# Performance work log

Hardware: AMD Instinct MI355X
Metric: run time of the kernel (lower is better)

Reference implementation:

```python
import jax, jax.numpy as jnp
import numpy as np

TEMPERATURE = 0.5

def setup_inputs() -> dict:
    key = jax.random.key(0)
    k1, k2 = jax.random.split(key)
    N, D = 4096, 256
    return {
        "z_i": jax.random.normal(k1, (N, D), dtype=jnp.float32),
        "z_j": jax.random.normal(k2, (N, D), dtype=jnp.float32),
    }

def reference(z_i, z_j):
    N = z_i.shape[0]
    z = jnp.concatenate([z_i, z_j], axis=0)                      # [2N, D]
    # cosine similarity via normalize + GEMM (same math as broadcasted CosineSimilarity)
    zn = z / jnp.linalg.norm(z, axis=-1, keepdims=True)
    sim = (zn @ zn.T) / TEMPERATURE                              # [2N, 2N]
    twoN = 2 * N
    eye = jnp.eye(twoN, dtype=bool)
    labels = jnp.arange(N, dtype=jnp.int32)
    labels = jnp.concatenate([labels, labels])
    pos_mask = (labels[None, :] == labels[:, None]) & (~eye)     # positive pairs, no diagonal
    # removing the diagonal before exp == zeroing exp on the diagonal
    exps = jnp.where(eye, 0.0, jnp.exp(sim))                     # [2N, 2N]
    pos = jnp.sum(jnp.where(pos_mask, exps, 0.0), axis=1)        # [2N]
    denom = jnp.sum(exps, axis=1)                                # [2N]
    loss = -jnp.mean(jnp.log(pos / denom))
    return loss
```

## Files before the change

kernel.cpp:

```cpp
#include <hip/hip_runtime.h>
#include <hip/hip_bf16.h>
#include <hip/hip_fp8.h>

#define TWO_N 8192
#define NHALF 4096
#define D 256
#define NTILE 64
#define BLK_BYTES 32768
static constexpr float INV_T = 2.0f;

typedef __attribute__((ext_vector_type(4))) float f32x4;

#define AS1 __attribute__((address_space(1)))
#define AS3 __attribute__((address_space(3)))

__device__ __forceinline__ unsigned int pack4_e4m3(float a, float b, float c, float d) {
#if __has_builtin(__builtin_amdgcn_cvt_pk_fp8_f32)
    int p = 0;
    p = __builtin_amdgcn_cvt_pk_fp8_f32(a, b, p, false);
    p = __builtin_amdgcn_cvt_pk_fp8_f32(c, d, p, true);
    return (unsigned int)p;
#else
    __hip_fp8_e4m3 qa(a), qb(b), qc(c), qd(d);
    return (unsigned int)qa.__x | ((unsigned int)qb.__x << 8) |
           ((unsigned int)qc.__x << 16) | ((unsigned int)qd.__x << 24);
#endif
}

__global__ __launch_bounds__(256) void norm_pos_kernel(
        const float* __restrict__ z_i, const float* __restrict__ z_j,
        unsigned char* __restrict__ znb, float* __restrict__ sim_pos,
        float* __restrict__ denom) {
    const int wid = threadIdx.x >> 6, lane = threadIdx.x & 63;
    const int i = blockIdx.x * 4 + wid;
    const float4 vi = *reinterpret_cast<const float4*>(z_i + (size_t)i * D + lane * 4);
    const float4 vj = *reinterpret_cast<const float4*>(z_j + (size_t)i * D + lane * 4);
    float ssi = vi.x * vi.x + vi.y * vi.y + vi.z * vi.z + vi.w * vi.w;
    float ssj = vj.x * vj.x + vj.y * vj.y + vj.z * vj.z + vj.w * vj.w;
    float dt  = vi.x * vj.x + vi.y * vj.y + vi.z * vj.z + vi.w * vj.w;
    #pragma unroll
    for (int off = 32; off; off >>= 1) {
        ssi += __shfl_xor(ssi, off);
        ssj += __shfl_xor(ssj, off);
        dt  += __shfl_xor(dt,  off);
    }
    const float ri = rsqrtf(ssi), rj = rsqrtf(ssj);
    const unsigned int pi = pack4_e4m3(vi.x * ri, vi.y * ri, vi.z * ri, vi.w * ri);
    const unsigned int pj = pack4_e4m3(vj.x * rj, vj.y * rj, vj.z * rj, vj.w * rj);
    const size_t sub = (size_t)(lane >> 3) * 4096 + (size_t)((lane >> 1) & 3) * 1024
                     + (size_t)(i & 127) * 8 + (lane & 1) * 4;
    const int i2 = i + NHALF;
    *reinterpret_cast<unsigned int*>(znb + (size_t)(i  >> 7) * BLK_BYTES + sub) = pi;
    *reinterpret_cast<unsigned int*>(znb + (size_t)(i2 >> 7) * BLK_BYTES + sub) = pj;
    if (lane == 0) {
        const float sp = dt * ri * rj * INV_T;
        sim_pos[i] = sp;
        sim_pos[i + NHALF] = sp;
        denom[i] = 0.0f;
        denom[i + NHALF] = 0.0f;
    }
}

__global__ __launch_bounds__(256) void gemm_denom_kernel(
        const unsigned char* __restrict__ znb, float* __restrict__ denom) {
    const int tr = blockIdx.x;
    const int tc = blockIdx.y;
    if (tc < tr) return;

    __shared__ unsigned char As[3][4096];
    __shared__ unsigned char Bs[3][4096];

    const int tid  = threadIdx.x;
    const int lane = tid & 63;
    const int wid  = tid >> 6;
    const int wr   = wid >> 1;
    const int wc   = wid & 1;
    const int r16  = lane & 15;
    const int kgrp = lane >> 4;
    const int row0 = tr * 128;
    const int col0 = tc * 128;

    const unsigned char* gA = znb + (size_t)tr * BLK_BYTES + tid * 16;
    const unsigned char* gB = znb + (size_t)tc * BLK_BYTES + tid * 16;
    const int dst = wid * 1024;

    #define STAGE(buf, koff)                                                      \
        do {                                                                      \
            __builtin_amdgcn_global_load_lds((const AS1 void*)(gA + (koff)),      \
                (AS3 void*)(As[buf] + dst), 16, 0, 0);                            \
            __builtin_amdgcn_global_load_lds((const AS1 void*)(gB + (koff)),      \
                (AS3 void*)(Bs[buf] + dst), 16, 0, 0);                            \
        } while (0)

    f32x4 acc[4][4];
    #pragma unroll
    for (int m = 0; m < 4; ++m)
        #pragma unroll
        for (int n = 0; n < 4; ++n) {
            f32x4 z = {0.f, 0.f, 0.f, 0.f};
            acc[m][n] = z;
        }

    STAGE(0, 0);
    STAGE(1, 4096);

    #pragma unroll
    for (int ks = 0; ks < 8; ++ks) {
        const int cur = ks % 3;
        if (ks < 7) asm volatile("s_waitcnt vmcnt(2)" ::: "memory");
        else        asm volatile("s_waitcnt vmcnt(0)" ::: "memory");
        __builtin_amdgcn_s_barrier();
        asm volatile("" ::: "memory");
        if (ks < 6) STAGE((ks + 2) % 3, (ks + 2) * 4096);
        long a[4], b[4];
        #pragma unroll
        for (int m = 0; m < 4; ++m)
            a[m] = *reinterpret_cast<const long*>(
                As[cur] + kgrp * 1024 + (wr * 64 + m * 16 + r16) * 8);
        #pragma unroll
        for (int n = 0; n < 4; ++n)
            b[n] = *reinterpret_cast<const long*>(
                Bs[cur] + kgrp * 1024 + (wc * 64 + n * 16 + r16) * 8);
        #pragma unroll
        for (int m = 0; m < 4; ++m)
            #pragma unroll
            for (int n = 0; n < 4; ++n)
                acc[m][n] = __builtin_amdgcn_mfma_f32_16x16x32_fp8_fp8(
                    a[m], b[n], acc[m][n], 0, 0, 0);
    }
    #undef STAGE

    const bool offdiag = (tr != tc);
    float cs[4] = {0.f, 0.f, 0.f, 0.f};
    #pragma unroll
    for (int m = 0; m < 4; ++m) {
        #pragma unroll
        for (int reg = 0; reg < 4; ++reg) {
            const int rg = row0 + wr * 64 + m * 16 + kgrp * 4 + reg;
            float rs = 0.f;
            #pragma unroll
            for (int n = 0; n < 4; ++n) {
                const int cg = col0 + wc * 64 + n * 16 + r16;
                float e = __expf(acc[m][n][reg] * INV_T);
                if (rg == cg) e = 0.f;
                rs += e;
                cs[n] += e;
            }
            rs += __shfl_xor(rs, 1);
            rs += __shfl_xor(rs, 2);
            rs += __shfl_xor(rs, 4);
            rs += __shfl_xor(rs, 8);
            if (r16 == 0) atomicAdd(&denom[rg], rs);
        }
    }
    if (offdiag) {
        #pragma unroll
        for (int n = 0; n < 4; ++n) {
            cs[n] += __shfl_xor(cs[n], 16);
            cs[n] += __shfl_xor(cs[n], 32);
        }
        if (kgrp == 0) {
            #pragma unroll
            for (int n = 0; n < 4; ++n)
                atomicAdd(&denom[col0 + wc * 64 + n * 16 + r16], cs[n]);
        }
    }
}

__global__ __launch_bounds__(1024) void final_kernel(
        const float* __restrict__ sim_pos, const float* __restrict__ denom,
        float* __restrict__ out) {
    const int tid = threadIdx.x;
    float s = 0.f;
    for (int i = tid; i < TWO_N; i += 1024)
        s += sim_pos[i] - logf(denom[i]);
    #pragma unroll
    for (int off = 32; off; off >>= 1) s += __shfl_down(s, off);
    __shared__ float red[16];
    const int wid = tid >> 6, lane = tid & 63;
    if (lane == 0) red[wid] = s;
    __syncthreads();
    if (tid == 0) {
        float t = 0.f;
        #pragma unroll
        for (int w = 0; w < 16; ++w) t += red[w];
        out[0] = -t / (float)TWO_N;
    }
}

extern "C" void kernel_launch(void* const* d_in, const int* in_sizes, int n_in,
                              void* d_out, int out_size, void* d_ws, size_t ws_size,
                              hipStream_t stream) {
    const float* z_i = (const float*)d_in[0];
    const float* z_j = (const float*)d_in[1];
    float* out = (float*)d_out;

    unsigned char* znb = (unsigned char*)d_ws;
    float* sim_pos = (float*)((char*)d_ws + (size_t)TWO_N * D * 2);
    float* denom   = sim_pos + TWO_N;

    norm_pos_kernel<<<NHALF / 4, 256, 0, stream>>>(z_i, z_j, znb, sim_pos, denom);
    dim3 grid(NTILE, NTILE);
    gemm_denom_kernel<<<grid, 256, 0, stream>>>(znb, denom);
    final_kernel<<<1, 1024, 0, stream>>>(sim_pos, denom, out);
}
```

Measured before the change: 49.76 us.

## Double GEMM k-step depth and parallelize final reduction across blocks

The fp8 block layout is regrouped so each pipeline stage covers 64 k-bytes instead of 32. The GEMM loop then runs 4 iterations with two MFMA sub-steps each, halving barriers and waitcnt points at the cost of doubled LDS buffers. The final log-sum kernel now runs 8 blocks that combine through an atomic accumulator and a ticket counter, both reset in the norm kernel. The intent is to cut per-iteration synchronisation overhead and the serial tail of the single-block reduction.

```diff
diff --git a/kernel.cpp b/kernel.cpp
--- a/kernel.cpp
+++ b/kernel.cpp
@@ -30,9 +30,11 @@
 __global__ __launch_bounds__(256) void norm_pos_kernel(
         const float* __restrict__ z_i, const float* __restrict__ z_j,
         unsigned char* __restrict__ znb, float* __restrict__ sim_pos,
-        float* __restrict__ denom) {
+        float* __restrict__ denom, float* __restrict__ facc,
+        int* __restrict__ ftick) {
     const int wid = threadIdx.x >> 6, lane = threadIdx.x & 63;
     const int i = blockIdx.x * 4 + wid;
+    if (blockIdx.x == 0 && threadIdx.x == 0) { facc[0] = 0.0f; ftick[0] = 0; }
     const float4 vi = *reinterpret_cast<const float4*>(z_i + (size_t)i * D + lane * 4);
     const float4 vj = *reinterpret_cast<const float4*>(z_j + (size_t)i * D + lane * 4);
     float ssi = vi.x * vi.x + vi.y * vi.y + vi.z * vi.z + vi.w * vi.w;
@@ -47,7 +49,7 @@
     const float ri = rsqrtf(ssi), rj = rsqrtf(ssj);
     const unsigned int pi = pack4_e4m3(vi.x * ri, vi.y * ri, vi.z * ri, vi.w * ri);
     const unsigned int pj = pack4_e4m3(vj.x * rj, vj.y * rj, vj.z * rj, vj.w * rj);
-    const size_t sub = (size_t)(lane >> 3) * 4096 + (size_t)((lane >> 1) & 3) * 1024
+    const size_t sub = (size_t)(lane >> 4) * 8192 + (size_t)((lane >> 1) & 7) * 1024
                      + (size_t)(i & 127) * 8 + (lane & 1) * 4;
     const int i2 = i + NHALF;
     *reinterpret_cast<unsigned int*>(znb + (size_t)(i  >> 7) * BLK_BYTES + sub) = pi;
@@ -67,8 +69,8 @@
     const int tc = blockIdx.y;
     if (tc < tr) return;
 
-    __shared__ unsigned char As[3][4096];
-    __shared__ unsigned char Bs[3][4096];
+    __shared__ unsigned char As[3][8192];
+    __shared__ unsigned char Bs[3][8192];
 
     const int tid  = threadIdx.x;
     const int lane = tid & 63;
@@ -88,8 +90,12 @@
         do {                                                                      \
             __builtin_amdgcn_global_load_lds((const AS1 void*)(gA + (koff)),      \
                 (AS3 void*)(As[buf] + dst), 16, 0, 0);                            \
+            __builtin_amdgcn_global_load_lds((const AS1 void*)(gA + (koff) + 4096),\
+                (AS3 void*)(As[buf] + 4096 + dst), 16, 0, 0);                     \
             __builtin_amdgcn_global_load_lds((const AS1 void*)(gB + (koff)),      \
                 (AS3 void*)(Bs[buf] + dst), 16, 0, 0);                            \
+            __builtin_amdgcn_global_load_lds((const AS1 void*)(gB + (koff) + 4096),\
+                (AS3 void*)(Bs[buf] + 4096 + dst), 16, 0, 0);                     \
         } while (0)
 
     f32x4 acc[4][4];
@@ -102,31 +108,34 @@
         }
 
     STAGE(0, 0);
-    STAGE(1, 4096);
-
-    #pragma unroll
-    for (int ks = 0; ks < 8; ++ks) {
+    STAGE(1, 8192);
+
+    #pragma unroll
+    for (int ks = 0; ks < 4; ++ks) {
         const int cur = ks % 3;
-        if (ks < 7) asm volatile("s_waitcnt vmcnt(2)" ::: "memory");
+        if (ks < 3) asm volatile("s_waitcnt vmcnt(8)" ::: "memory");
         else        asm volatile("s_waitcnt vmcnt(0)" ::: "memory");
         __builtin_amdgcn_s_barrier();
         asm volatile("" ::: "memory");
-        if (ks < 6) STAGE((ks + 2) % 3, (ks + 2) * 4096);
-        long a[4], b[4];
-        #pragma unroll
-        for (int m = 0; m < 4; ++m)
-            a[m] = *reinterpret_cast<const long*>(
-                As[cur] + kgrp * 1024 + (wr * 64 + m * 16 + r16) * 8);
-        #pragma unroll
-        for (int n = 0; n < 4; ++n)
-            b[n] = *reinterpret_cast<const long*>(
-                Bs[cur] + kgrp * 1024 + (wc * 64 + n * 16 + r16) * 8);
-        #pragma unroll
-        for (int m = 0; m < 4; ++m)
+        if (ks < 2) STAGE((ks + 2) % 3, (ks + 2) * 8192);
+        #pragma unroll
+        for (int s = 0; s < 2; ++s) {
+            long a[4], b[4];
+            #pragma unroll
+            for (int m = 0; m < 4; ++m)
+                a[m] = *reinterpret_cast<const long*>(
+                    As[cur] + (((s * 4 + kgrp) * 128) + wr * 64 + m * 16 + r16) * 8);
             #pragma unroll
             for (int n = 0; n < 4; ++n)
-                acc[m][n] = __builtin_amdgcn_mfma_f32_16x16x32_fp8_fp8(
-                    a[m], b[n], acc[m][n], 0, 0, 0);
+                b[n] = *reinterpret_cast<const long*>(
+                    Bs[cur] + (((s * 4 + kgrp) * 128) + wc * 64 + n * 16 + r16) * 8);
+            #pragma unroll
+            for (int m = 0; m < 4; ++m)
+                #pragma unroll
+                for (int n = 0; n < 4; ++n)
+                    acc[m][n] = __builtin_amdgcn_mfma_f32_16x16x32_fp8_fp8(
+                        a[m], b[n], acc[m][n], 0, 0, 0);
+        }
     }
     #undef STAGE
 
@@ -169,11 +178,11 @@
 
 __global__ __launch_bounds__(1024) void final_kernel(
         const float* __restrict__ sim_pos, const float* __restrict__ denom,
+        float* __restrict__ facc, int* __restrict__ ftick,
         float* __restrict__ out) {
     const int tid = threadIdx.x;
-    float s = 0.f;
-    for (int i = tid; i < TWO_N; i += 1024)
-        s += sim_pos[i] - logf(denom[i]);
+    const int gid = blockIdx.x * 1024 + tid;
+    float s = sim_pos[gid] - __logf(denom[gid]);
     #pragma unroll
     for (int off = 32; off; off >>= 1) s += __shfl_down(s, off);
     __shared__ float red[16];
@@ -181,10 +190,16 @@
     if (lane == 0) red[wid] = s;
     __syncthreads();
     if (tid == 0) {
-        float t = 0.f;
-        #pragma unroll
-        for (int w = 0; w < 16; ++w) t += red[w];
-        out[0] = -t / (float)TWO_N;
+        float bs = 0.f;
+        #pragma unroll
+        for (int w = 0; w < 16; ++w) bs += red[w];
+        atomicAdd(facc, bs);
+        __threadfence();
+        const int t = atomicAdd(ftick, 1);
+        if (t == 7) {
+            const float tot = atomicAdd(facc, 0.0f);
+            out[0] = -tot / (float)TWO_N;
+        }
     }
 }
 
@@ -198,9 +213,12 @@
     unsigned char* znb = (unsigned char*)d_ws;
     float* sim_pos = (float*)((char*)d_ws + (size_t)TWO_N * D * 2);
     float* denom   = sim_pos + TWO_N;
-
-    norm_pos_kernel<<<NHALF / 4, 256, 0, stream>>>(z_i, z_j, znb, sim_pos, denom);
+    float* facc    = denom + TWO_N;
+    int*   ftick   = (int*)(facc + 1);
+
+    norm_pos_kernel<<<NHALF / 4, 256, 0, stream>>>(z_i, z_j, znb, sim_pos, denom,
+                                                   facc, ftick);
     dim3 grid(NTILE, NTILE);
     gemm_denom_kernel<<<grid, 256, 0, stream>>>(znb, denom);
-    final_kernel<<<1, 1024, 0, stream>>>(sim_pos, denom, out);
-}
+    final_kernel<<<TWO_N / 1024, 1024, 0, stream>>>(sim_pos, denom, facc, ftick, out);
+}
```

Result: faster. 47.25 us (-5.0%).
